# Performance work log

Measured on AMD Instinct MI355X. Metric: run time of the kernel, lower is better.

## Reference

```python
import jax, jax.numpy as jnp
import numpy as np
import math

B, N, IN_DIM, OUT_DIM, H = 8, 1024, 256, 256, 8
D_K = OUT_DIM // H


def setup_inputs() -> dict:
    key = jax.random.key(0)
    ks = jax.random.split(key, 12)
    s_in = 1.0 / math.sqrt(IN_DIM)
    s_out = 1.0 / math.sqrt(OUT_DIM)
    return {
        "X": jax.random.normal(ks[0], (B, N, IN_DIM), jnp.float32),
        "A": jax.random.randint(ks[1], (B, N, N), 0, 2, jnp.int32),
        "D": jax.random.uniform(ks[2], (B, N, N), jnp.float32),
        "W_q": jax.random.uniform(ks[3], (IN_DIM, OUT_DIM), jnp.float32, -s_in, s_in),
        "b_q": jax.random.uniform(ks[4], (OUT_DIM,), jnp.float32, -s_in, s_in),
        "W_k": jax.random.uniform(ks[5], (IN_DIM, OUT_DIM), jnp.float32, -s_in, s_in),
        "b_k": jax.random.uniform(ks[6], (OUT_DIM,), jnp.float32, -s_in, s_in),
        "W_v": jax.random.uniform(ks[7], (IN_DIM, OUT_DIM), jnp.float32, -s_in, s_in),
        "b_v": jax.random.uniform(ks[8], (OUT_DIM,), jnp.float32, -s_in, s_in),
        "W_o": jax.random.uniform(ks[9], (OUT_DIM, OUT_DIM), jnp.float32, -s_out, s_out),
        "b_o": jax.random.uniform(ks[10], (OUT_DIM,), jnp.float32, -s_out, s_out),
        "dist_scale": jnp.array(1.0, jnp.float32),
    }


def reference(X, A, D, W_q, b_q, W_k, b_k, W_v, b_v, W_o, b_o, dist_scale):
    b, n, _ = X.shape
    # Projections -> [B, H, N, d_k]
    Q = (X @ W_q + b_q).reshape(b, n, H, D_K).transpose(0, 2, 1, 3)
    K = (X @ W_k + b_k).reshape(b, n, H, D_K).transpose(0, 2, 1, 3)
    V = (X @ W_v + b_v).reshape(b, n, H, D_K).transpose(0, 2, 1, 3)
    scores = jnp.einsum("bhqd,bhkd->bhqk", Q, K) / jnp.sqrt(jnp.float32(D_K))
    scores = scores - dist_scale * D[:, None, :, :]
    scores = jnp.where(A[:, None, :, :] <= 0, jnp.float32(-1e9), scores)
    attn = jax.nn.softmax(scores, axis=-1)  # dropout is identity in eval mode
    out = jnp.einsum("bhqk,bhkd->bhqd", attn, V)
    out = out.transpose(0, 2, 1, 3).reshape(b, n, H * D_K)
    return out @ W_o + b_o
```

## Files before the change

### kernel.cpp

```cpp
#include <hip/hip_runtime.h>


typedef _Float16 f16x8 __attribute__((ext_vector_type(8)));
typedef __fp16 h16x2 __attribute__((ext_vector_type(2)));
typedef float f32x4 __attribute__((ext_vector_type(4)));
typedef int i32x4 __attribute__((ext_vector_type(4)));
typedef unsigned short u16x8 __attribute__((ext_vector_type(8)));

#define DEV static __device__ __forceinline__

#define LOG2E 1.4426950408889634f
#define QSCALE 0.2550351062f

DEV unsigned short f2h(float f) {
  _Float16 h = (_Float16)f;
  unsigned short u;
  __builtin_memcpy(&u, &h, 2);
  return u;
}

DEV f32x4 mfma16h(f16x8 a, f16x8 b, f32x4 c) {
  return __builtin_amdgcn_mfma_f32_16x16x32_f16(a, b, c, 0, 0, 0);
}

DEV f16x8 ldfragh(const unsigned short* p) {
  return *reinterpret_cast<const f16x8*>(p);
}

__global__ __launch_bounds__(256) void k_prep(
    const float* __restrict__ X, const int* __restrict__ A,
    const float* __restrict__ D, const float* __restrict__ dscale,
    const float* __restrict__ Wq, const float* __restrict__ Wk,
    const float* __restrict__ Wv, const float* __restrict__ Wo,
    unsigned short* __restrict__ Xh, unsigned short* __restrict__ Wt,
    unsigned short* __restrict__ Bias) {
  const int tid = blockIdx.x * 256 + threadIdx.x;
  const int NB4 = (8 * 1024 * 1024) / 4;
  const int NX4 = (8192 * 256) / 4;
  if (tid < NB4) {
    const i32x4 a4 = reinterpret_cast<const i32x4*>(A)[tid];
    const f32x4 d4 = reinterpret_cast<const f32x4*>(D)[tid];
    const float c = -dscale[0] * LOG2E;
    ushort4 o;
    unsigned short* op = (unsigned short*)&o;
    #pragma unroll
    for (int i = 0; i < 4; ++i)
      op[i] = f2h(a4[i] <= 0 ? -60000.0f : c * d4[i]);
    reinterpret_cast<ushort4*>(Bias)[tid] = o;
  } else if (tid < NB4 + NX4) {
    const int t = tid - NB4;
    float4 v = reinterpret_cast<const float4*>(X)[t];
    union { h16x2 h2[2]; ushort4 u; } o;
    o.h2[0] = __builtin_amdgcn_cvt_pkrtz(v.x, v.y);
    o.h2[1] = __builtin_amdgcn_cvt_pkrtz(v.z, v.w);
    reinterpret_cast<ushort4*>(Xh)[t] = o.u;
  } else {
    int t = tid - NB4 - NX4;
    int mat = t >> 16;
    int e = t & 65535;
    int n = e >> 8, k = e & 255;
    const float* W = (mat == 0) ? Wq : (mat == 1) ? Wk : (mat == 2) ? Wv : Wo;
    Wt[t] = f2h(W[k * 256 + n]);
  }
}

__global__ __launch_bounds__(256, 2) void k_qkv(
    const unsigned short* __restrict__ Xh, const unsigned short* __restrict__ Wt,
    const float* __restrict__ bq, const float* __restrict__ bk,
    const float* __restrict__ bv,
    unsigned short* __restrict__ Qb, unsigned short* __restrict__ Kb,
    unsigned short* __restrict__ Vt) {
  const int lane = threadIdx.x & 63;
  const int w = threadIdx.x >> 6;
  const int lr = lane & 15, lg = lane >> 4;
  const int mat = blockIdx.y >> 2;
  const int nloc = (blockIdx.y & 3) * 64 + w * 16;
  const int mbase = blockIdx.x << 8;

  const unsigned short* Wm = Wt + mat * 65536;
  const float* bias = (mat == 0) ? bq : (mat == 1) ? bk : bv;

  f16x8 bfr[8];
  #pragma unroll
  for (int ks = 0; ks < 8; ++ks)
    bfr[ks] = ldfragh(Wm + (nloc + lr) * 256 + ks * 32 + lg * 8);
  const float bb = bias[nloc + lr];
  const int cm = nloc + lr;
  const int hh = cm >> 5, d = cm & 31;

  for (int mt = 0; mt < 16; ++mt) {
    const int m0 = mbase + mt * 16;
    f16x8 a[8];
    #pragma unroll
    for (int ks = 0; ks < 8; ++ks)
      a[ks] = ldfragh(Xh + (m0 + lr) * 256 + ks * 32 + lg * 8);
    f32x4 acc = {0.f, 0.f, 0.f, 0.f};
    #pragma unroll
    for (int ks = 0; ks < 8; ++ks)
      acc = mfma16h(a[ks], bfr[ks], acc);

    if (mat == 2) {
      union { h16x2 h2[2]; ushort4 u; } vv;
      vv.h2[0] = __builtin_amdgcn_cvt_pkrtz(acc[0] + bb, acc[1] + bb);
      vv.h2[1] = __builtin_amdgcn_cvt_pkrtz(acc[2] + bb, acc[3] + bb);
      const int row = m0 + lg * 4;
      const int bidx = row >> 10, nn = row & 1023;
      *reinterpret_cast<ushort4*>(&Vt[(((bidx * 8 + hh) * 32) + d) * 1024 + nn]) = vv.u;
    } else if (mat == 0) {
      #pragma unroll
      for (int i = 0; i < 4; ++i) {
        const int row = m0 + lg * 4 + i;
        const int bidx = row >> 10, nn = row & 1023;
        Qb[(((bidx * 8 + hh) * 1024) + nn) * 32 + d] = f2h((acc[i] + bb) * QSCALE);
      }
    } else {
      #pragma unroll
      for (int i = 0; i < 4; ++i) {
        const int row = m0 + lg * 4 + i;
        const int bidx = row >> 10, nn = row & 1023;
        Kb[(((bidx * 8 + hh) * 1024) + nn) * 32 + d] = f2h(acc[i] + bb);
      }
    }
  }
}

__global__ __launch_bounds__(512, 2) void k_attn(
    const unsigned short* __restrict__ Qb, const unsigned short* __restrict__ Kb,
    const unsigned short* __restrict__ Vt, const unsigned short* __restrict__ Bias,
    unsigned short* __restrict__ AO) {
  __shared__ alignas(16) unsigned short Klds[1024 * 32];
  __shared__ alignas(16) unsigned short Vlds[32 * 1024];
  __shared__ alignas(16) unsigned short Sbuf[8][16][72];

  const int tid = threadIdx.x;
  const int lane = tid & 63;
  const int w = tid >> 6;
  const int lr = lane & 15, lg = lane >> 4;
  const int bi = blockIdx.x;
  const int b = bi & 7;
  const int j = bi >> 3;
  const int h = j >> 2, qq = j & 3;
  const int q0w = qq * 256 + w * 32;

  const unsigned short* Kg = Kb + ((size_t)(b * 8 + h) << 15);
  const unsigned short* Vg = Vt + ((size_t)(b * 8 + h) << 15);
  const unsigned short* Qh = Qb + ((size_t)(b * 8 + h) << 15);

  #pragma unroll
  for (int p = 0; p < 8; ++p) {
    const int c = tid + p * 512;
    const int row = c >> 2, seg = c & 3;
    const u16x8 v = *reinterpret_cast<const u16x8*>(Kg + c * 8);
    *reinterpret_cast<u16x8*>(&Klds[row * 32 + ((seg ^ (row & 3)) << 3)]) = v;
  }
  #pragma unroll
  for (int p = 0; p < 8; ++p) {
    const int c = tid + p * 512;
    const int row = c >> 7, ch = c & 127;
    const u16x8 v = *reinterpret_cast<const u16x8*>(Vg + c * 8);
    *reinterpret_cast<u16x8*>(&Vlds[row * 1024 + ((ch ^ (row & 7)) << 3)]) = v;
  }

  f16x8 qf[2];
  qf[0] = ldfragh(Qh + (q0w + lr) * 32 + lg * 8);
  qf[1] = ldfragh(Qh + (q0w + 16 + lr) * 32 + lg * 8);
  const unsigned short* Br0 = Bias + ((size_t)b << 20) + (size_t)(q0w + lr) * 1024;
  const unsigned short* Br1 = Br0 + (size_t)16 * 1024;

  u16x8 bc[2][2], bn[2][2];
  #pragma unroll
  for (int fr = 0; fr < 2; ++fr) {
    bc[0][fr] = *reinterpret_cast<const u16x8*>(Br0 + fr * 32 + lg * 8);
    bc[1][fr] = *reinterpret_cast<const u16x8*>(Br1 + fr * 32 + lg * 8);
  }

  __syncthreads();

  f32x4 o[2][2];
  f32x4 lacc[2];
  #pragma unroll
  for (int s = 0; s < 2; ++s) {
    #pragma unroll
    for (int dh = 0; dh < 2; ++dh) o[s][dh] = f32x4{0.f, 0.f, 0.f, 0.f};
    lacc[s] = f32x4{0.f, 0.f, 0.f, 0.f};
  }
  f16x8 onesv;
  #pragma unroll
  for (int i = 0; i < 8; ++i) onesv[i] = (_Float16)1.0f;

  for (int t = 0; t < 16; ++t) {
    const int k0 = t << 6;
    if (t < 15) {
      #pragma unroll
      for (int fr = 0; fr < 2; ++fr) {
        bn[0][fr] = *reinterpret_cast<const u16x8*>(Br0 + k0 + 64 + fr * 32 + lg * 8);
        bn[1][fr] = *reinterpret_cast<const u16x8*>(Br1 + k0 + 64 + fr * 32 + lg * 8);
      }
    }

    f16x8 kf[4];
    #pragma unroll
    for (int st = 0; st < 4; ++st) {
      const int row = k0 + st * 16 + lr;
      kf[st] = *reinterpret_cast<const f16x8*>(
          &Klds[row * 32 + ((lg ^ (lr & 3)) << 3)]);
    }
    f16x8 vf[2][2];
    #pragma unroll
    for (int dh = 0; dh < 2; ++dh)
      #pragma unroll
      for (int fr = 0; fr < 2; ++fr) {
        const int row = dh * 16 + lr;
        const int ch = t * 8 + ((fr * 4 + lg) ^ (lr & 7));
        vf[dh][fr] = *reinterpret_cast<const f16x8*>(&Vlds[row * 1024 + ch * 8]);
      }

    #pragma unroll
    for (int s = 0; s < 2; ++s) {
      const f32x4 zz = {0.f, 0.f, 0.f, 0.f};
      f32x4 sv[4];
      #pragma unroll
      for (int st = 0; st < 4; ++st)
        sv[st] = mfma16h(kf[st], qf[s], zz);

      #pragma unroll
      for (int st = 0; st < 4; ++st) {
        union { h16x2 h2[2]; ushort4 u; } sw;
        sw.h2[0] = __builtin_amdgcn_cvt_pkrtz(sv[st][0], sv[st][1]);
        sw.h2[1] = __builtin_amdgcn_cvt_pkrtz(sv[st][2], sv[st][3]);
        *reinterpret_cast<ushort4*>(&Sbuf[w][lr][st * 16 + lg * 4]) = sw.u;
      }

      #pragma unroll
      for (int fr = 0; fr < 2; ++fr) {
        const f16x8 sf = *reinterpret_cast<const f16x8*>(&Sbuf[w][lr][fr * 32 + lg * 8]);
        const f16x8 bfv = *reinterpret_cast<const f16x8*>(&bc[s][fr]);
        const f16x8 sb = sf + bfv;
        float e[8];
        #pragma unroll
        for (int i = 0; i < 8; ++i) e[i] = exp2f((float)sb[i]);
        union { h16x2 h2[4]; f16x8 v; } pfu;
        #pragma unroll
        for (int i = 0; i < 4; ++i)
          pfu.h2[i] = __builtin_amdgcn_cvt_pkrtz(e[2 * i], e[2 * i + 1]);
        const f16x8 pf = pfu.v;
        o[s][0] = mfma16h(vf[0][fr], pf, o[s][0]);
        o[s][1] = mfma16h(vf[1][fr], pf, o[s][1]);
        lacc[s] = mfma16h(onesv, pf, lacc[s]);
      }
    }

    #pragma unroll
    for (int s = 0; s < 2; ++s)
      #pragma unroll
      for (int fr = 0; fr < 2; ++fr)
        bc[s][fr] = bn[s][fr];
  }

  #pragma unroll
  for (int s = 0; s < 2; ++s) {
    const float linv = 1.0f / lacc[s][0];
    ushort4 r0, r1;
    unsigned short* r0p = (unsigned short*)&r0;
    unsigned short* r1p = (unsigned short*)&r1;
    #pragma unroll
    for (int i = 0; i < 4; ++i) {
      r0p[i] = f2h(o[s][0][i] * linv);
      r1p[i] = f2h(o[s][1][i] * linv);
    }
    const int row = (b << 10) + q0w + s * 16 + lr;
    *reinterpret_cast<ushort4*>(&AO[row * 256 + h * 32 + lg * 4]) = r0;
    *reinterpret_cast<ushort4*>(&AO[row * 256 + h * 32 + 16 + lg * 4]) = r1;
  }
}

__global__ __launch_bounds__(256, 2) void k_oproj(
    const unsigned short* __restrict__ AO, const unsigned short* __restrict__ Wto,
    const float* __restrict__ bo, float* __restrict__ out) {
  const int lane = threadIdx.x & 63;
  const int w = threadIdx.x >> 6;
  const int lr = lane & 15, lg = lane >> 4;
  const int c0 = blockIdx.y * 64 + w * 16;
  const int mbase = blockIdx.x << 7;

  f16x8 bfr[8];
  #pragma unroll
  for (int ks = 0; ks < 8; ++ks)
    bfr[ks] = ldfragh(Wto + (c0 + lr) * 256 + ks * 32 + lg * 8);
  const float bb = bo[c0 + lr];

  for (int mt = 0; mt < 8; ++mt) {
    const int m0 = mbase + mt * 16;
    f16x8 a[8];
    #pragma unroll
    for (int ks = 0; ks < 8; ++ks)
      a[ks] = ldfragh(AO + (m0 + lr) * 256 + ks * 32 + lg * 8);
    f32x4 acc = {0.f, 0.f, 0.f, 0.f};
    #pragma unroll
    for (int ks = 0; ks < 8; ++ks)
      acc = mfma16h(a[ks], bfr[ks], acc);
    #pragma unroll
    for (int i = 0; i < 4; ++i) {
      const int row = m0 + lg * 4 + i;
      out[row * 256 + c0 + lr] = acc[i] + bb;
    }
  }
}

extern "C" void kernel_launch(void* const* d_in, const int* in_sizes, int n_in,
                              void* d_out, int out_size, void* d_ws, size_t ws_size,
                              hipStream_t stream) {
  const float* X   = (const float*)d_in[0];
  const int*   A   = (const int*)d_in[1];
  const float* D   = (const float*)d_in[2];
  const float* Wq  = (const float*)d_in[3];
  const float* bq  = (const float*)d_in[4];
  const float* Wk  = (const float*)d_in[5];
  const float* bk  = (const float*)d_in[6];
  const float* Wv  = (const float*)d_in[7];
  const float* bv  = (const float*)d_in[8];
  const float* Wo  = (const float*)d_in[9];
  const float* bo  = (const float*)d_in[10];
  const float* dsc = (const float*)d_in[11];
  float* out = (float*)d_out;

  unsigned short* ws = (unsigned short*)d_ws;
  unsigned short* Xh   = ws;
  unsigned short* Wt   = ws + 2097152;
  unsigned short* Qb   = ws + 2359296;
  unsigned short* Kb   = ws + 4456448;
  unsigned short* Vt   = ws + 6553600;
  unsigned short* Bias = ws + 8650752;
  unsigned short* AO   = Xh;

  hipLaunchKernelGGL(k_prep, dim3(11264), dim3(256), 0, stream,
                     X, A, D, dsc, Wq, Wk, Wv, Wo, Xh, Wt, Bias);
  hipLaunchKernelGGL(k_qkv, dim3(32, 12), dim3(256), 0, stream,
                     Xh, Wt, bq, bk, bv, Qb, Kb, Vt);
  hipLaunchKernelGGL(k_attn, dim3(256), dim3(512), 0, stream,
                     Qb, Kb, Vt, Bias, AO);
  hipLaunchKernelGGL(k_oproj, dim3(64, 4), dim3(256), 0, stream,
                     AO, Wt + 196608, bo, out);
}
```

Before: 88.91 us.

## Split attention blocks to 16 queries per wave and stream K/V in chunks

The attention kernel now launches twice as many blocks, each wave handling 16 query rows instead of 32. K and V are staged through LDS in four 256-key chunks instead of the full 1024-key sequence, which shrinks shared memory per block and raises the launch-bounds occupancy target. This aims to fill all CUs (512 blocks vs 256) and let more waves hide latency. The cost is that each K/V tile is loaded by twice as many blocks and each chunk adds extra barriers.

```diff
diff --git a/kernel.cpp b/kernel.cpp
--- a/kernel.cpp
+++ b/kernel.cpp
@@ -124,12 +124,12 @@
   }
 }
 
-__global__ __launch_bounds__(512, 2) void k_attn(
+__global__ __launch_bounds__(512, 4) void k_attn(
     const unsigned short* __restrict__ Qb, const unsigned short* __restrict__ Kb,
     const unsigned short* __restrict__ Vt, const unsigned short* __restrict__ Bias,
     unsigned short* __restrict__ AO) {
-  __shared__ alignas(16) unsigned short Klds[1024 * 32];
-  __shared__ alignas(16) unsigned short Vlds[32 * 1024];
+  __shared__ alignas(16) unsigned short Klds[256 * 32];
+  __shared__ alignas(16) unsigned short Vlds[32 * 256];
   __shared__ alignas(16) unsigned short Sbuf[8][16][72];
 
   const int tid = threadIdx.x;
@@ -139,89 +139,77 @@
   const int bi = blockIdx.x;
   const int b = bi & 7;
   const int j = bi >> 3;
-  const int h = j >> 2, qq = j & 3;
-  const int q0w = qq * 256 + w * 32;
+  const int h = j >> 3, qe = j & 7;
+  const int q0w = qe * 128 + w * 16;
 
   const unsigned short* Kg = Kb + ((size_t)(b * 8 + h) << 15);
   const unsigned short* Vg = Vt + ((size_t)(b * 8 + h) << 15);
   const unsigned short* Qh = Qb + ((size_t)(b * 8 + h) << 15);
 
-  #pragma unroll
-  for (int p = 0; p < 8; ++p) {
-    const int c = tid + p * 512;
-    const int row = c >> 2, seg = c & 3;
-    const u16x8 v = *reinterpret_cast<const u16x8*>(Kg + c * 8);
-    *reinterpret_cast<u16x8*>(&Klds[row * 32 + ((seg ^ (row & 3)) << 3)]) = v;
-  }
-  #pragma unroll
-  for (int p = 0; p < 8; ++p) {
-    const int c = tid + p * 512;
-    const int row = c >> 7, ch = c & 127;
-    const u16x8 v = *reinterpret_cast<const u16x8*>(Vg + c * 8);
-    *reinterpret_cast<u16x8*>(&Vlds[row * 1024 + ((ch ^ (row & 7)) << 3)]) = v;
-  }
-
-  f16x8 qf[2];
-  qf[0] = ldfragh(Qh + (q0w + lr) * 32 + lg * 8);
-  qf[1] = ldfragh(Qh + (q0w + 16 + lr) * 32 + lg * 8);
-  const unsigned short* Br0 = Bias + ((size_t)b << 20) + (size_t)(q0w + lr) * 1024;
-  const unsigned short* Br1 = Br0 + (size_t)16 * 1024;
-
-  u16x8 bc[2][2], bn[2][2];
-  #pragma unroll
-  for (int fr = 0; fr < 2; ++fr) {
-    bc[0][fr] = *reinterpret_cast<const u16x8*>(Br0 + fr * 32 + lg * 8);
-    bc[1][fr] = *reinterpret_cast<const u16x8*>(Br1 + fr * 32 + lg * 8);
-  }
-
-  __syncthreads();
-
-  f32x4 o[2][2];
-  f32x4 lacc[2];
-  #pragma unroll
-  for (int s = 0; s < 2; ++s) {
-    #pragma unroll
-    for (int dh = 0; dh < 2; ++dh) o[s][dh] = f32x4{0.f, 0.f, 0.f, 0.f};
-    lacc[s] = f32x4{0.f, 0.f, 0.f, 0.f};
-  }
+  const f16x8 qf = ldfragh(Qh + (q0w + lr) * 32 + lg * 8);
+  const unsigned short* Br0 = Bias + ((size_t)b << 20) + (size_t)(q0w + lr) * 1024
+                              + lg * 8;
+
+  u16x8 bc[2], bn[2];
+  #pragma unroll
+  for (int fr = 0; fr < 2; ++fr)
+    bc[fr] = *reinterpret_cast<const u16x8*>(Br0 + fr * 32);
+
+  f32x4 o0 = {0.f, 0.f, 0.f, 0.f}, o1 = {0.f, 0.f, 0.f, 0.f};
+  f32x4 lacc = {0.f, 0.f, 0.f, 0.f};
   f16x8 onesv;
   #pragma unroll
   for (int i = 0; i < 8; ++i) onesv[i] = (_Float16)1.0f;
 
-  for (int t = 0; t < 16; ++t) {
-    const int k0 = t << 6;
-    if (t < 15) {
-      #pragma unroll
-      for (int fr = 0; fr < 2; ++fr) {
-        bn[0][fr] = *reinterpret_cast<const u16x8*>(Br0 + k0 + 64 + fr * 32 + lg * 8);
-        bn[1][fr] = *reinterpret_cast<const u16x8*>(Br1 + k0 + 64 + fr * 32 + lg * 8);
-      }
-    }
-
-    f16x8 kf[4];
-    #pragma unroll
-    for (int st = 0; st < 4; ++st) {
-      const int row = k0 + st * 16 + lr;
-      kf[st] = *reinterpret_cast<const f16x8*>(
-          &Klds[row * 32 + ((lg ^ (lr & 3)) << 3)]);
-    }
-    f16x8 vf[2][2];
-    #pragma unroll
-    for (int dh = 0; dh < 2; ++dh)
-      #pragma unroll
-      for (int fr = 0; fr < 2; ++fr) {
-        const int row = dh * 16 + lr;
-        const int ch = t * 8 + ((fr * 4 + lg) ^ (lr & 7));
-        vf[dh][fr] = *reinterpret_cast<const f16x8*>(&Vlds[row * 1024 + ch * 8]);
-      }
-
-    #pragma unroll
-    for (int s = 0; s < 2; ++s) {
+  for (int qt = 0; qt < 4; ++qt) {
+    __syncthreads();
+    #pragma unroll
+    for (int p = 0; p < 2; ++p) {
+      const int c = tid + p * 512;
+      const int row = c >> 2, seg = c & 3;
+      const u16x8 v = *reinterpret_cast<const u16x8*>(Kg + qt * 8192 + c * 8);
+      *reinterpret_cast<u16x8*>(&Klds[row * 32 + ((seg ^ (row & 3)) << 3)]) = v;
+    }
+    #pragma unroll
+    for (int p = 0; p < 2; ++p) {
+      const int c = tid + p * 512;
+      const int row = c >> 5, ch = c & 31;
+      const u16x8 v = *reinterpret_cast<const u16x8*>(Vg + row * 1024 + qt * 256 + ch * 8);
+      *reinterpret_cast<u16x8*>(&Vlds[row * 256 + ((ch ^ (row & 7)) << 3)]) = v;
+    }
+    __syncthreads();
+
+    #pragma unroll
+    for (int t = 0; t < 4; ++t) {
+      const int g = qt * 4 + t;
+      if (g < 15) {
+        #pragma unroll
+        for (int fr = 0; fr < 2; ++fr)
+          bn[fr] = *reinterpret_cast<const u16x8*>(Br0 + (g + 1) * 64 + fr * 32);
+      }
+
+      f16x8 kf[4];
+      #pragma unroll
+      for (int st = 0; st < 4; ++st) {
+        const int row = t * 64 + st * 16 + lr;
+        kf[st] = *reinterpret_cast<const f16x8*>(
+            &Klds[row * 32 + ((lg ^ (lr & 3)) << 3)]);
+      }
+      f16x8 vf[2][2];
+      #pragma unroll
+      for (int dh = 0; dh < 2; ++dh)
+        #pragma unroll
+        for (int fr = 0; fr < 2; ++fr) {
+          const int row = dh * 16 + lr;
+          const int ch = t * 8 + ((fr * 4 + lg) ^ (lr & 7));
+          vf[dh][fr] = *reinterpret_cast<const f16x8*>(&Vlds[row * 256 + ch * 8]);
+        }
+
       const f32x4 zz = {0.f, 0.f, 0.f, 0.f};
       f32x4 sv[4];
       #pragma unroll
       for (int st = 0; st < 4; ++st)
-        sv[st] = mfma16h(kf[st], qf[s], zz);
+        sv[st] = mfma16h(kf[st], qf, zz);
 
       #pragma unroll
       for (int st = 0; st < 4; ++st) {
@@ -234,7 +222,7 @@
       #pragma unroll
       for (int fr = 0; fr < 2; ++fr) {
         const f16x8 sf = *reinterpret_cast<const f16x8*>(&Sbuf[w][lr][fr * 32 + lg * 8]);
-        const f16x8 bfv = *reinterpret_cast<const f16x8*>(&bc[s][fr]);
+        const f16x8 bfv = *reinterpret_cast<const f16x8*>(&bc[fr]);
         const f16x8 sb = sf + bfv;
         float e[8];
         #pragma unroll
@@ -244,34 +232,28 @@
         for (int i = 0; i < 4; ++i)
           pfu.h2[i] = __builtin_amdgcn_cvt_pkrtz(e[2 * i], e[2 * i + 1]);
         const f16x8 pf = pfu.v;
-        o[s][0] = mfma16h(vf[0][fr], pf, o[s][0]);
-        o[s][1] = mfma16h(vf[1][fr], pf, o[s][1]);
-        lacc[s] = mfma16h(onesv, pf, lacc[s]);
-      }
-    }
-
-    #pragma unroll
-    for (int s = 0; s < 2; ++s)
-      #pragma unroll
-      for (int fr = 0; fr < 2; ++fr)
-        bc[s][fr] = bn[s][fr];
-  }
-
-  #pragma unroll
-  for (int s = 0; s < 2; ++s) {
-    const float linv = 1.0f / lacc[s][0];
-    ushort4 r0, r1;
-    unsigned short* r0p = (unsigned short*)&r0;
-    unsigned short* r1p = (unsigned short*)&r1;
-    #pragma unroll
-    for (int i = 0; i < 4; ++i) {
-      r0p[i] = f2h(o[s][0][i] * linv);
-      r1p[i] = f2h(o[s][1][i] * linv);
-    }
-    const int row = (b << 10) + q0w + s * 16 + lr;
-    *reinterpret_cast<ushort4*>(&AO[row * 256 + h * 32 + lg * 4]) = r0;
-    *reinterpret_cast<ushort4*>(&AO[row * 256 + h * 32 + 16 + lg * 4]) = r1;
-  }
+        o0 = mfma16h(vf[0][fr], pf, o0);
+        o1 = mfma16h(vf[1][fr], pf, o1);
+        lacc = mfma16h(onesv, pf, lacc);
+      }
+
+      #pragma unroll
+      for (int fr = 0; fr < 2; ++fr) bc[fr] = bn[fr];
+    }
+  }
+
+  const float linv = 1.0f / lacc[0];
+  ushort4 r0, r1;
+  unsigned short* r0p = (unsigned short*)&r0;
+  unsigned short* r1p = (unsigned short*)&r1;
+  #pragma unroll
+  for (int i = 0; i < 4; ++i) {
+    r0p[i] = f2h(o0[i] * linv);
+    r1p[i] = f2h(o1[i] * linv);
+  }
+  const int row = (b << 10) + q0w + lr;
+  *reinterpret_cast<ushort4*>(&AO[row * 256 + h * 32 + lg * 4]) = r0;
+  *reinterpret_cast<ushort4*>(&AO[row * 256 + h * 32 + 16 + lg * 4]) = r1;
 }
 
 __global__ __launch_bounds__(256, 2) void k_oproj(
@@ -337,7 +319,7 @@
                      X, A, D, dsc, Wq, Wk, Wv, Wo, Xh, Wt, Bias);
   hipLaunchKernelGGL(k_qkv, dim3(32, 12), dim3(256), 0, stream,
                      Xh, Wt, bq, bk, bv, Qb, Kb, Vt);
-  hipLaunchKernelGGL(k_attn, dim3(256), dim3(512), 0, stream,
+  hipLaunchKernelGGL(k_attn, dim3(512), dim3(512), 0, stream,
                      Qb, Kb, Vt, Bias, AO);
   hipLaunchKernelGGL(k_oproj, dim3(64, 4), dim3(256), 0, stream,
                      AO, Wt + 196608, bo, out);
```

Measured after the change: 91.76 us. 3.2% more time.
